# Performance work log

Hardware: AMD Instinct MI355X
Metric: run time of the kernel (lower is better)

The kernel has to match this reference:

```python
import jax, jax.numpy as jnp
import numpy as np

V, E, H, B, L = 50000, 256, 512, 128, 512
T = 9
START, STOP = 7, 8
H2 = H // 2
NEG = -10000.0


def _lstm_dir(x, h0, c0, Wih, Whh, bih, bhh, reverse):
    # x: [B, L, E]; PyTorch gate order i, f, g, o
    def step(carry, xt):
        h, c = carry
        z = xt @ Wih.T + bih + h @ Whh.T + bhh  # [B, 4*H2]
        i, f, g, o = jnp.split(z, 4, axis=-1)
        i = jax.nn.sigmoid(i)
        f = jax.nn.sigmoid(f)
        g = jnp.tanh(g)
        o = jax.nn.sigmoid(o)
        c = f * c + i * g
        h = o * jnp.tanh(c)
        return (h, c), h

    _, hs = jax.lax.scan(step, (h0, c0), x.transpose(1, 0, 2), reverse=reverse)
    return hs.transpose(1, 0, 2)  # [B, L, H2]


def _viterbi(feats, transitions):
    # feats: [B, L, T]; transitions[i, j] = score of j -> i
    alpha0 = jnp.full((B, T), NEG, dtype=feats.dtype).at[:, START].set(0.0)

    def step(alpha, feat):
        # smat[b, prev, nxt] = alpha[b, prev] + feat[b, nxt] + transitions[nxt, prev]
        smat = alpha[:, :, None] + feat[:, None, :] + transitions.T[None]
        return smat.max(axis=1), smat.argmax(axis=1)  # new alpha [B,T], bptr [B,T]

    alpha, backtrace = jax.lax.scan(step, alpha0, feats.transpose(1, 0, 2))  # backtrace: [L, B, T]
    final = alpha + transitions[STOP][None, :]  # [B, T]
    best_score = final.max(axis=1)
    last_tag = final.argmax(axis=1)  # [B]

    def back_step(tag, bptr):
        prev = jnp.take_along_axis(bptr, tag[:, None], axis=1)[:, 0]
        return prev, prev

    # torch loop skips backtrace[0] (points to START)
    _, tags = jax.lax.scan(back_step, last_tag, backtrace[1:], reverse=True)  # [L-1, B]
    path = jnp.concatenate([tags.T, last_tag[:, None]], axis=1)  # [B, L]
    return best_score, path


def setup_inputs():
    key = jax.random.key(0)
    ks = jax.random.split(key, 16)
    s = 0.05
    trans = jax.random.normal(ks[12], (T, T), dtype=jnp.float32)
    trans = trans.at[START, :].set(NEG).at[:, STOP].set(NEG)
    return {
        "tokens": jax.random.randint(ks[0], (B, L), 0, V),
        "embedding": jax.random.normal(ks[1], (V, E), dtype=jnp.float32) * s,
        "Wih_f": jax.random.normal(ks[2], (4 * H2, E), dtype=jnp.float32) * s,
        "Whh_f": jax.random.normal(ks[3], (4 * H2, H2), dtype=jnp.float32) * s,
        "bih_f": jnp.zeros((4 * H2,), dtype=jnp.float32),
        "bhh_f": jnp.zeros((4 * H2,), dtype=jnp.float32),
        "Wih_b": jax.random.normal(ks[4], (4 * H2, E), dtype=jnp.float32) * s,
        "Whh_b": jax.random.normal(ks[5], (4 * H2, H2), dtype=jnp.float32) * s,
        "bih_b": jnp.zeros((4 * H2,), dtype=jnp.float32),
        "bhh_b": jnp.zeros((4 * H2,), dtype=jnp.float32),
        "W_out": jax.random.normal(ks[6], (T, H), dtype=jnp.float32) * s,
        "b_out": jnp.zeros((T,), dtype=jnp.float32),
        "transitions": trans,
        "h0": jax.random.normal(ks[7], (2, B, H2), dtype=jnp.float32),
        "c0": jax.random.normal(ks[8], (2, B, H2), dtype=jnp.float32),
    }


def reference(tokens, embedding, Wih_f, Whh_f, bih_f, bhh_f, Wih_b, Whh_b, bih_b, bhh_b,
              W_out, b_out, transitions, h0, c0):
    x = embedding[tokens]  # [B, L, E]
    hf = _lstm_dir(x, h0[0], c0[0], Wih_f, Whh_f, bih_f, bhh_f, reverse=False)
    hb = _lstm_dir(x, h0[1], c0[1], Wih_b, Whh_b, bih_b, bhh_b, reverse=True)
    lstm_out = jnp.concatenate([hf, hb], axis=-1)  # [B, L, H]
    feats = lstm_out @ W_out.T + b_out  # [B, L, T]
    best_score, path = _viterbi(feats, transitions)
    return best_score, path
```

## Files before the change

kernel.cpp:

```cpp
#include <hip/hip_runtime.h>
#include <hip/hip_bf16.h>
#include <math.h>

#define NB   128
#define LSEQ 512
#define EE   256
#define HH2  256
#define HHH  512
#define TT   9
#define START_TAG 7
#define STOP_TAG  8
#define NEGV -10000.0f

#define ABUF_BYTES 65536
#define ZROW 34
#define LDS_BYTES (ABUF_BYTES + 4 * 32 * ZROW * 4)

#define XFRAG_BYTES  ((size_t)LSEQ * 4 * 16 * 64 * 16)
#define HFRAG_BYTES  ((size_t)LSEQ * 2 * 4 * 16 * 64 * 16)
#define HPLAIN_BYTES ((size_t)LSEQ * NB * HHH * 2)
#define FEATS_BYTES  ((size_t)LSEQ * NB * TT * 4)
#define OFF_HFRAG  XFRAG_BYTES
#define OFF_HPLAIN (OFF_HFRAG + HFRAG_BYTES)
#define OFF_FEATS  (OFF_HPLAIN + HPLAIN_BYTES)
#define OFF_FLAGS  (OFF_FEATS + FEATS_BYTES)

typedef float f32x16 __attribute__((ext_vector_type(16)));
typedef short short8 __attribute__((ext_vector_type(8)));

static __device__ __forceinline__ unsigned short f2bf(float f) {
  unsigned int u = __float_as_uint(f);
  unsigned int r = (u + 0x7fffu + ((u >> 16) & 1u)) >> 16;
  return (unsigned short)r;
}
static __device__ __forceinline__ float bf2f(unsigned short s) {
  return __uint_as_float(((unsigned int)s) << 16);
}
static __device__ __forceinline__ float sigmoidf_(float x) {
  return 1.0f / (1.0f + __expf(-x));
}
static __device__ __forceinline__ float tanhf_(float x) {
  return 2.0f / (1.0f + __expf(-2.0f * x)) - 1.0f;
}

__global__ void init_kernel(unsigned int* flags) {
  if (threadIdx.x < 64) flags[threadIdx.x] = 0u;
}

__global__ void embed_kernel(const int* __restrict__ tokens,
                             const float* __restrict__ emb,
                             uint4* __restrict__ x_frag) {
  int wid = blockIdx.x * blockDim.x + threadIdx.x;
  int l  = wid & 63;
  int ks = (wid >> 6) & 15;
  int bt = (wid >> 10) & 3;
  int t  = wid >> 12;
  int b  = bt * 32 + (l & 31);
  int k  = ks * 16 + (l >> 5) * 8;
  int tok = tokens[b * LSEQ + t];
  const float* p = emb + (size_t)tok * EE + k;
  float4 v0 = *(const float4*)p;
  float4 v1 = *(const float4*)(p + 4);
  uint4 o;
  o.x = f2bf(v0.x) | ((unsigned)f2bf(v0.y) << 16);
  o.y = f2bf(v0.z) | ((unsigned)f2bf(v0.w) << 16);
  o.z = f2bf(v1.x) | ((unsigned)f2bf(v1.y) << 16);
  o.w = f2bf(v1.z) | ((unsigned)f2bf(v1.w) << 16);
  x_frag[wid] = o;
}

__global__ __launch_bounds__(256, 1)
void lstm_kernel(const uint4* __restrict__ x_frag,
                 const float* __restrict__ Wih_f, const float* __restrict__ Whh_f,
                 const float* __restrict__ bih_f, const float* __restrict__ bhh_f,
                 const float* __restrict__ Wih_b, const float* __restrict__ Whh_b,
                 const float* __restrict__ bih_b, const float* __restrict__ bhh_b,
                 const float* __restrict__ h0, const float* __restrict__ c0,
                 uint4* __restrict__ h_frag, ushort* __restrict__ h_plain,
                 unsigned int* __restrict__ flags) {
  extern __shared__ char smem[];
  char*  abuf = smem;
  float* zbuf = (float*)(smem + ABUF_BYTES);

  const int tid  = threadIdx.x;
  const int wv   = tid >> 6;
  const int lane = tid & 63;
  const int d  = blockIdx.x >> 5;
  const int bt = (blockIdx.x >> 3) & 3;
  const int ut = blockIdx.x & 7;
  const int grp = d * 4 + bt;

  const float* Wih = d ? Wih_b : Wih_f;
  const float* Whh = d ? Whh_b : Whh_f;
  const float* bih = d ? bih_b : bih_f;
  const float* bhh = d ? bhh_b : bhh_f;

  short8 w[32];
  {
    int wrow = wv * 256 + ut * 32 + (lane & 31);
#pragma unroll
    for (int ks = 0; ks < 32; ++ks) {
      int k0 = ks * 16 + (lane >> 5) * 8;
      const float* src = (k0 < 256) ? (Wih + (size_t)wrow * 256 + k0)
                                    : (Whh + (size_t)wrow * 256 + (k0 - 256));
      float4 v0 = *(const float4*)src;
      float4 v1 = *(const float4*)(src + 4);
      short8 s;
      s[0] = (short)f2bf(v0.x); s[1] = (short)f2bf(v0.y);
      s[2] = (short)f2bf(v0.z); s[3] = (short)f2bf(v0.w);
      s[4] = (short)f2bf(v1.x); s[5] = (short)f2bf(v1.y);
      s[6] = (short)f2bf(v1.z); s[7] = (short)f2bf(v1.w);
      w[ks] = s;
    }
  }

  const int uj = tid >> 6;
  const int ul = tid & 63;
  const int ubl = ul & 31;
  const int u0l = 16 * uj + 8 * (ul >> 5);
  const int bg  = bt * 32 + ubl;
  const int ug  = ut * 32 + u0l;
  float creg[8];
  float bias[4][8];
  if (tid < 128) {
    const float* cp = c0 + ((size_t)d * NB + bg) * HH2 + ug;
    float4 cv0 = *(const float4*)cp;
    float4 cv1 = *(const float4*)(cp + 4);
    creg[0]=cv0.x; creg[1]=cv0.y; creg[2]=cv0.z; creg[3]=cv0.w;
    creg[4]=cv1.x; creg[5]=cv1.y; creg[6]=cv1.z; creg[7]=cv1.w;
#pragma unroll
    for (int g = 0; g < 4; ++g) {
      int gr = g * 256 + ug;
      float4 a0 = *(const float4*)(bih + gr);
      float4 a1 = *(const float4*)(bih + gr + 4);
      float4 b0 = *(const float4*)(bhh + gr);
      float4 b1 = *(const float4*)(bhh + gr + 4);
      bias[g][0]=a0.x+b0.x; bias[g][1]=a0.y+b0.y; bias[g][2]=a0.z+b0.z; bias[g][3]=a0.w+b0.w;
      bias[g][4]=a1.x+b1.x; bias[g][5]=a1.y+b1.y; bias[g][6]=a1.z+b1.z; bias[g][7]=a1.w+b1.w;
    }
  }

  auto stage_x = [&](int tsrc) {
#pragma unroll
    for (int i = 0; i < 4; ++i) {
      int ks = wv * 4 + i;
      const char* gp = (const char*)x_frag +
          ((((size_t)tsrc * 4 + bt) * 16 + ks) * 64 + lane) * 16;
      char* lp = abuf + (((tsrc & 1) * 32 + ks) * 1024);
      __builtin_amdgcn_global_load_lds(
          (const __attribute__((address_space(1))) unsigned int*)gp,
          (__attribute__((address_space(3))) unsigned int*)lp, 16, 0, 0);
    }
  };
  auto stage_h = [&](int tsrc, int buf) {
#pragma unroll
    for (int i = 0; i < 4; ++i) {
      int ks2 = wv * 4 + i;
      const char* gp = (const char*)h_frag +
          (((((size_t)tsrc * 2 + d) * 4 + bt) * 16 + ks2) * 64 + lane) * 16;
      char* lp = abuf + ((buf * 32 + 16 + ks2) * 1024);
      __builtin_amdgcn_global_load_lds(
          (const __attribute__((address_space(1))) unsigned int*)gp,
          (__attribute__((address_space(3))) unsigned int*)lp, 16, 0, 0);
    }
  };

  stage_x(0);
#pragma unroll
  for (int w2 = 0; w2 < 4; ++w2) {
    int wid = w2 * 256 + tid;
    int ks2 = wid >> 6;
    int l2  = wid & 63;
    int u   = ks2 * 16 + (l2 >> 5) * 8;
    int b2  = bt * 32 + (l2 & 31);
    const float* p = h0 + ((size_t)d * NB + b2) * HH2 + u;
    float4 v0 = *(const float4*)p;
    float4 v1 = *(const float4*)(p + 4);
    uint4 o;
    o.x = f2bf(v0.x) | ((unsigned)f2bf(v0.y) << 16);
    o.y = f2bf(v0.z) | ((unsigned)f2bf(v0.w) << 16);
    o.z = f2bf(v1.x) | ((unsigned)f2bf(v1.y) << 16);
    o.w = f2bf(v1.z) | ((unsigned)f2bf(v1.w) << 16);
    *(uint4*)(abuf + ((16 + ks2) * 1024) + l2 * 16) = o;
  }
  asm volatile("s_waitcnt vmcnt(0)" ::: "memory");
  __syncthreads();

  for (int t = 0; t < LSEQ; ++t) {
    const int cur = t & 1;
    if (t + 1 < LSEQ) stage_x(t + 1);
    if (t > 0) {
      const unsigned int tgt = (unsigned int)t;
      while (true) {
        unsigned int v = __hip_atomic_load(&flags[grp * 8 + (tid & 7)],
                                           __ATOMIC_RELAXED, __HIP_MEMORY_SCOPE_AGENT);
        if (__all(v >= tgt)) break;
        __builtin_amdgcn_s_sleep(1);
      }
      stage_h(t - 1, cur);
    }

    f32x16 acc0, acc1;
#pragma unroll
    for (int i = 0; i < 16; ++i) { acc0[i] = 0.0f; acc1[i] = 0.0f; }

#pragma unroll
    for (int ks = 0; ks < 16; ks += 2) {
      short8 a0 = *(const short8*)(abuf + ((cur * 32 + ks) * 1024) + lane * 16);
      short8 a1 = *(const short8*)(abuf + ((cur * 32 + ks + 1) * 1024) + lane * 16);
      asm volatile("v_mfma_f32_32x32x16_bf16 %0, %1, %2, %0"
                   : "+v"(acc0) : "v"(a0), "v"(w[ks]));
      asm volatile("v_mfma_f32_32x32x16_bf16 %0, %1, %2, %0"
                   : "+v"(acc1) : "v"(a1), "v"(w[ks + 1]));
    }
    asm volatile("s_waitcnt vmcnt(0)" ::: "memory");
    __syncthreads();
#pragma unroll
    for (int ks = 16; ks < 32; ks += 2) {
      short8 a0 = *(const short8*)(abuf + ((cur * 32 + ks) * 1024) + lane * 16);
      short8 a1 = *(const short8*)(abuf + ((cur * 32 + ks + 1) * 1024) + lane * 16);
      asm volatile("v_mfma_f32_32x32x16_bf16 %0, %1, %2, %0"
                   : "+v"(acc0) : "v"(a0), "v"(w[ks]));
      asm volatile("v_mfma_f32_32x32x16_bf16 %0, %1, %2, %0"
                   : "+v"(acc1) : "v"(a1), "v"(w[ks + 1]));
    }
#pragma unroll
    for (int i = 0; i < 16; ++i) acc0[i] += acc1[i];

#pragma unroll
    for (int r = 0; r < 16; ++r) {
      int brow = (r & 3) + 8 * (r >> 2) + 4 * (lane >> 5);
      zbuf[(wv * 32 + brow) * ZROW + (lane & 31)] = acc0[r];
    }
    __syncthreads();

    if (tid < 128) {
      float zr[4][8];
#pragma unroll
      for (int g = 0; g < 4; ++g) {
        const float* zp = zbuf + (g * 32 + ubl) * ZROW + u0l;
        float2 p0 = *(const float2*)zp;
        float2 p1 = *(const float2*)(zp + 2);
        float2 p2 = *(const float2*)(zp + 4);
        float2 p3 = *(const float2*)(zp + 6);
        zr[g][0]=p0.x; zr[g][1]=p0.y; zr[g][2]=p1.x; zr[g][3]=p1.y;
        zr[g][4]=p2.x; zr[g][5]=p2.y; zr[g][6]=p3.x; zr[g][7]=p3.y;
      }
      unsigned short hb[8];
#pragma unroll
      for (int e = 0; e < 8; ++e) {
        float ig = sigmoidf_(zr[0][e] + bias[0][e]);
        float fg = sigmoidf_(zr[1][e] + bias[1][e]);
        float gg = tanhf_   (zr[2][e] + bias[2][e]);
        float og = sigmoidf_(zr[3][e] + bias[3][e]);
        float c = fg * creg[e] + ig * gg;
        creg[e] = c;
        hb[e] = f2bf(og * tanhf_(c));
      }
      int tt = d ? (LSEQ - 1 - t) : t;
      size_t fo = ((((size_t)tt * 2 + d) * 4 + bt) * 16 + (2 * ut + uj)) * 64 + ul;
      unsigned long long w0 = (unsigned long long)(hb[0] | ((unsigned)hb[1] << 16)) |
                              ((unsigned long long)(hb[2] | ((unsigned)hb[3] << 16)) << 32);
      unsigned long long w1 = (unsigned long long)(hb[4] | ((unsigned)hb[5] << 16)) |
                              ((unsigned long long)(hb[6] | ((unsigned)hb[7] << 16)) << 32);
      unsigned long long* fp = (unsigned long long*)((char*)h_frag + fo * 16);
      __hip_atomic_store(fp,     w0, __ATOMIC_RELAXED, __HIP_MEMORY_SCOPE_AGENT);
      __hip_atomic_store(fp + 1, w1, __ATOMIC_RELAXED, __HIP_MEMORY_SCOPE_AGENT);
      uint4 hp;
      hp.x = hb[0] | ((unsigned)hb[1] << 16);
      hp.y = hb[2] | ((unsigned)hb[3] << 16);
      hp.z = hb[4] | ((unsigned)hb[5] << 16);
      hp.w = hb[6] | ((unsigned)hb[7] << 16);
      *(uint4*)(h_plain + (((size_t)tt * NB + bg) * HHH) + d * HH2 + ug) = hp;
    }
    asm volatile("s_waitcnt vmcnt(0)" ::: "memory");
    __syncthreads();
    if (tid == 0)
      __hip_atomic_store(&flags[grp * 8 + ut], (unsigned int)(t + 1),
                         __ATOMIC_RELAXED, __HIP_MEMORY_SCOPE_AGENT);
  }
}

__global__ __launch_bounds__(256)
void feats_kernel(const ushort* __restrict__ h_plain,
                  const float* __restrict__ W_out, const float* __restrict__ b_out,
                  float* __restrict__ feats) {
  int wv = threadIdx.x >> 6, lane = threadIdx.x & 63;
  int wid = blockIdx.x * 4 + wv;
  const ushort* hrow = h_plain + (size_t)wid * HHH + lane * 8;
  uint4 hv = *(const uint4*)hrow;
  float hf[8];
  hf[0] = __uint_as_float(hv.x << 16); hf[1] = __uint_as_float(hv.x & 0xffff0000u);
  hf[2] = __uint_as_float(hv.y << 16); hf[3] = __uint_as_float(hv.y & 0xffff0000u);
  hf[4] = __uint_as_float(hv.z << 16); hf[5] = __uint_as_float(hv.z & 0xffff0000u);
  hf[6] = __uint_as_float(hv.w << 16); hf[7] = __uint_as_float(hv.w & 0xffff0000u);
#pragma unroll
  for (int tg = 0; tg < TT; ++tg) {
    const float* wrow = W_out + (size_t)tg * HHH + lane * 8;
    float4 w0 = *(const float4*)wrow;
    float4 w1 = *(const float4*)(wrow + 4);
    float s = hf[0]*w0.x + hf[1]*w0.y + hf[2]*w0.z + hf[3]*w0.w
            + hf[4]*w1.x + hf[5]*w1.y + hf[6]*w1.z + hf[7]*w1.w;
#pragma unroll
    for (int off = 32; off >= 1; off >>= 1) s += __shfl_xor(s, off);
    if (lane == 0) feats[(size_t)wid * TT + tg] = s + b_out[tg];
  }
}

__global__ __launch_bounds__(64)
void viterbi_kernel(const float* __restrict__ feats, const float* __restrict__ trans,
                    float* __restrict__ out) {
  __shared__ float tr[TT * TT];
  __shared__ float abuf2[2][16];
  __shared__ int   bptr[LSEQ][TT];
  __shared__ float finbuf[16];
  int b = blockIdx.x, lane = threadIdx.x;
  for (int i = lane; i < TT * TT; i += 64) tr[i] = trans[i];
  if (lane < 16) abuf2[0][lane] = NEGV;
  __syncthreads();
  if (lane == START_TAG) abuf2[0][lane] = 0.f;
  int cur = 0;
  for (int l = 0; l < LSEQ; ++l) {
    float feat = (lane < TT) ? feats[((size_t)l * NB + b) * TT + lane] : 0.f;
    if (lane < TT) {
      float best = -3.4e38f; int bp = 0;
#pragma unroll
      for (int p = 0; p < TT; ++p) {
        float s2 = abuf2[cur][p] + tr[lane * TT + p];
        if (s2 > best) { best = s2; bp = p; }
      }
      abuf2[cur ^ 1][lane] = best + feat;
      bptr[l][lane] = bp;
    }
    cur ^= 1;
  }
  if (lane < 16) finbuf[lane] = -3.4e38f;
  if (lane < TT) finbuf[lane] = abuf2[cur][lane] + tr[STOP_TAG * TT + lane];
  if (lane == 0) {
    float bestv = finbuf[0]; int btag = 0;
    for (int p = 1; p < TT; ++p) if (finbuf[p] > bestv) { bestv = finbuf[p]; btag = p; }
    out[b] = bestv;
    float* pathp = out + NB + (size_t)b * LSEQ;
    int tag = btag;
    pathp[LSEQ - 1] = (float)tag;
    for (int l = LSEQ - 1; l >= 1; --l) {
      tag = bptr[l][tag];
      pathp[l - 1] = (float)tag;
    }
  }
}

extern "C" void kernel_launch(void* const* d_in, const int* in_sizes, int n_in,
                              void* d_out, int out_size, void* d_ws, size_t ws_size,
                              hipStream_t stream) {
  const int*   tokens = (const int*)d_in[0];
  const float* emb    = (const float*)d_in[1];
  const float* Wih_f  = (const float*)d_in[2];
  const float* Whh_f  = (const float*)d_in[3];
  const float* bih_f  = (const float*)d_in[4];
  const float* bhh_f  = (const float*)d_in[5];
  const float* Wih_b  = (const float*)d_in[6];
  const float* Whh_b  = (const float*)d_in[7];
  const float* bih_b  = (const float*)d_in[8];
  const float* bhh_b  = (const float*)d_in[9];
  const float* W_out  = (const float*)d_in[10];
  const float* b_out  = (const float*)d_in[11];
  const float* trans  = (const float*)d_in[12];
  const float* h0     = (const float*)d_in[13];
  const float* c0     = (const float*)d_in[14];
  float* out = (float*)d_out;

  char* ws = (char*)d_ws;
  uint4* x_frag  = (uint4*)ws;
  uint4* h_frag  = (uint4*)(ws + OFF_HFRAG);
  ushort* h_plain = (ushort*)(ws + OFF_HPLAIN);
  float* feats   = (float*)(ws + OFF_FEATS);
  unsigned int* flags = (unsigned int*)(ws + OFF_FLAGS);

  hipFuncSetAttribute((const void*)lstm_kernel,
                      hipFuncAttributeMaxDynamicSharedMemorySize, LDS_BYTES);

  init_kernel<<<1, 64, 0, stream>>>(flags);
  embed_kernel<<<(LSEQ * 4 * 16 * 64) / 256, 256, 0, stream>>>(tokens, emb, x_frag);
  lstm_kernel<<<64, 256, LDS_BYTES, stream>>>(x_frag, Wih_f, Whh_f, bih_f, bhh_f,
                                              Wih_b, Whh_b, bih_b, bhh_b,
                                              h0, c0, h_frag, h_plain, flags);
  feats_kernel<<<(LSEQ * NB) / 4, 256, 0, stream>>>(h_plain, W_out, b_out, feats);
  viterbi_kernel<<<NB, 64, 0, stream>>>(feats, trans, out);
}
```

Measured before the change: 2.575 ms.

## Halve LSTM blocks to 32 with 512 threads, fewer cross-block sync participants

The persistent LSTM kernel moves from 64 blocks of 256 threads to 32 blocks of 512 threads. Each block now covers 64 hidden units across all four gates, so every direction and batch group waits on 4 peer blocks per step instead of 8. Only one wave polls the flags, followed by a block barrier, and the h staging buffer is now single-buffered. The aim is to lower per-timestep grid synchronisation latency. The cost is an extra __syncthreads per step and fewer CUs doing the per-step matmul work.

```diff
diff --git a/kernel.cpp b/kernel.cpp
--- a/kernel.cpp
+++ b/kernel.cpp
@@ -12,9 +12,11 @@
 #define STOP_TAG  8
 #define NEGV -10000.0f
 
-#define ABUF_BYTES 65536
-#define ZROW 34
-#define LDS_BYTES (ABUF_BYTES + 4 * 32 * ZROW * 4)
+#define XBUF_BYTES 32768
+#define HBUF_OFF   XBUF_BYTES
+#define ZBUF_OFF   (XBUF_BYTES + 16384)
+#define ZROW 66
+#define LDS_BYTES (ZBUF_OFF + 4 * 32 * ZROW * 4)
 
 #define XFRAG_BYTES  ((size_t)LSEQ * 4 * 16 * 64 * 16)
 #define HFRAG_BYTES  ((size_t)LSEQ * 2 * 4 * 16 * 64 * 16)
@@ -24,6 +26,7 @@
 #define OFF_HPLAIN (OFF_HFRAG + HFRAG_BYTES)
 #define OFF_FEATS  (OFF_HPLAIN + HPLAIN_BYTES)
 #define OFF_FLAGS  (OFF_FEATS + FEATS_BYTES)
+#define FLAG_UINTS 128
 
 typedef float f32x16 __attribute__((ext_vector_type(16)));
 typedef short short8 __attribute__((ext_vector_type(8)));
@@ -33,9 +36,6 @@
   unsigned int r = (u + 0x7fffu + ((u >> 16) & 1u)) >> 16;
   return (unsigned short)r;
 }
-static __device__ __forceinline__ float bf2f(unsigned short s) {
-  return __uint_as_float(((unsigned int)s) << 16);
-}
 static __device__ __forceinline__ float sigmoidf_(float x) {
   return 1.0f / (1.0f + __expf(-x));
 }
@@ -44,7 +44,7 @@
 }
 
 __global__ void init_kernel(unsigned int* flags) {
-  if (threadIdx.x < 64) flags[threadIdx.x] = 0u;
+  if (threadIdx.x < FLAG_UINTS) flags[threadIdx.x] = 0u;
 }
 
 __global__ void embed_kernel(const int* __restrict__ tokens,
@@ -69,7 +69,7 @@
   x_frag[wid] = o;
 }
 
-__global__ __launch_bounds__(256, 1)
+__global__ __launch_bounds__(512, 2)
 void lstm_kernel(const uint4* __restrict__ x_frag,
                  const float* __restrict__ Wih_f, const float* __restrict__ Whh_f,
                  const float* __restrict__ bih_f, const float* __restrict__ bhh_f,
@@ -80,14 +80,16 @@
                  unsigned int* __restrict__ flags) {
   extern __shared__ char smem[];
   char*  abuf = smem;
-  float* zbuf = (float*)(smem + ABUF_BYTES);
+  float* zbuf = (float*)(smem + ZBUF_OFF);
 
   const int tid  = threadIdx.x;
   const int wv   = tid >> 6;
   const int lane = tid & 63;
-  const int d  = blockIdx.x >> 5;
-  const int bt = (blockIdx.x >> 3) & 3;
-  const int ut = blockIdx.x & 7;
+  const int gate = wv >> 1;
+  const int uh   = wv & 1;
+  const int d  = blockIdx.x >> 4;
+  const int bt = (blockIdx.x >> 2) & 3;
+  const int ut = blockIdx.x & 3;
   const int grp = d * 4 + bt;
 
   const float* Wih = d ? Wih_b : Wih_f;
@@ -97,7 +99,7 @@
 
   short8 w[32];
   {
-    int wrow = wv * 256 + ut * 32 + (lane & 31);
+    int wrow = gate * 256 + ut * 64 + uh * 32 + (lane & 31);
 #pragma unroll
     for (int ks = 0; ks < 32; ++ks) {
       int k0 = ks * 16 + (lane >> 5) * 8;
@@ -114,15 +116,13 @@
     }
   }
 
-  const int uj = tid >> 6;
-  const int ul = tid & 63;
-  const int ubl = ul & 31;
-  const int u0l = 16 * uj + 8 * (ul >> 5);
-  const int bg  = bt * 32 + ubl;
-  const int ug  = ut * 32 + u0l;
+  const int ub  = tid & 31;
+  const int un8 = tid >> 5;
+  const int bg  = bt * 32 + ub;
+  const int ug  = ut * 64 + un8 * 8;
   float creg[8];
   float bias[4][8];
-  if (tid < 128) {
+  if (tid < 256) {
     const float* cp = c0 + ((size_t)d * NB + bg) * HH2 + ug;
     float4 cv0 = *(const float4*)cp;
     float4 cv1 = *(const float4*)(cp + 4);
@@ -142,23 +142,23 @@
 
   auto stage_x = [&](int tsrc) {
 #pragma unroll
-    for (int i = 0; i < 4; ++i) {
-      int ks = wv * 4 + i;
+    for (int i = 0; i < 2; ++i) {
+      int ks = wv * 2 + i;
       const char* gp = (const char*)x_frag +
           ((((size_t)tsrc * 4 + bt) * 16 + ks) * 64 + lane) * 16;
-      char* lp = abuf + (((tsrc & 1) * 32 + ks) * 1024);
+      char* lp = abuf + (tsrc & 1) * 16384 + ks * 1024;
       __builtin_amdgcn_global_load_lds(
           (const __attribute__((address_space(1))) unsigned int*)gp,
           (__attribute__((address_space(3))) unsigned int*)lp, 16, 0, 0);
     }
   };
-  auto stage_h = [&](int tsrc, int buf) {
-#pragma unroll
-    for (int i = 0; i < 4; ++i) {
-      int ks2 = wv * 4 + i;
+  auto stage_h = [&](int tsrc) {
+#pragma unroll
+    for (int i = 0; i < 2; ++i) {
+      int ks = wv * 2 + i;
       const char* gp = (const char*)h_frag +
-          (((((size_t)tsrc * 2 + d) * 4 + bt) * 16 + ks2) * 64 + lane) * 16;
-      char* lp = abuf + ((buf * 32 + 16 + ks2) * 1024);
+          (((((size_t)tsrc * 2 + d) * 4 + bt) * 16 + ks) * 64 + lane) * 16;
+      char* lp = abuf + HBUF_OFF + ks * 1024;
       __builtin_amdgcn_global_load_lds(
           (const __attribute__((address_space(1))) unsigned int*)gp,
           (__attribute__((address_space(3))) unsigned int*)lp, 16, 0, 0);
@@ -167,8 +167,8 @@
 
   stage_x(0);
 #pragma unroll
-  for (int w2 = 0; w2 < 4; ++w2) {
-    int wid = w2 * 256 + tid;
+  for (int w2 = 0; w2 < 2; ++w2) {
+    int wid = w2 * 512 + tid;
     int ks2 = wid >> 6;
     int l2  = wid & 63;
     int u   = ks2 * 16 + (l2 >> 5) * 8;
@@ -181,7 +181,7 @@
     o.y = f2bf(v0.z) | ((unsigned)f2bf(v0.w) << 16);
     o.z = f2bf(v1.x) | ((unsigned)f2bf(v1.y) << 16);
     o.w = f2bf(v1.z) | ((unsigned)f2bf(v1.w) << 16);
-    *(uint4*)(abuf + ((16 + ks2) * 1024) + l2 * 16) = o;
+    *(uint4*)(abuf + HBUF_OFF + ks2 * 1024 + l2 * 16) = o;
   }
   asm volatile("s_waitcnt vmcnt(0)" ::: "memory");
   __syncthreads();
@@ -190,14 +190,17 @@
     const int cur = t & 1;
     if (t + 1 < LSEQ) stage_x(t + 1);
     if (t > 0) {
-      const unsigned int tgt = (unsigned int)t;
-      while (true) {
-        unsigned int v = __hip_atomic_load(&flags[grp * 8 + (tid & 7)],
-                                           __ATOMIC_RELAXED, __HIP_MEMORY_SCOPE_AGENT);
-        if (__all(v >= tgt)) break;
-        __builtin_amdgcn_s_sleep(1);
+      if (wv == 0) {
+        const unsigned int tgt = (unsigned int)t;
+        while (true) {
+          unsigned int v = __hip_atomic_load(&flags[grp * 16 + (lane & 3)],
+                                             __ATOMIC_RELAXED, __HIP_MEMORY_SCOPE_AGENT);
+          if (__all(v >= tgt)) break;
+          __builtin_amdgcn_s_sleep(1);
+        }
       }
-      stage_h(t - 1, cur);
+      __syncthreads();
+      stage_h(t - 1);
     }
 
     f32x16 acc0, acc1;
@@ -206,8 +209,8 @@
 
 #pragma unroll
     for (int ks = 0; ks < 16; ks += 2) {
-      short8 a0 = *(const short8*)(abuf + ((cur * 32 + ks) * 1024) + lane * 16);
-      short8 a1 = *(const short8*)(abuf + ((cur * 32 + ks + 1) * 1024) + lane * 16);
+      short8 a0 = *(const short8*)(abuf + cur * 16384 + ks * 1024 + lane * 16);
+      short8 a1 = *(const short8*)(abuf + cur * 16384 + (ks + 1) * 1024 + lane * 16);
       asm volatile("v_mfma_f32_32x32x16_bf16 %0, %1, %2, %0"
                    : "+v"(acc0) : "v"(a0), "v"(w[ks]));
       asm volatile("v_mfma_f32_32x32x16_bf16 %0, %1, %2, %0"
@@ -217,8 +220,8 @@
     __syncthreads();
 #pragma unroll
     for (int ks = 16; ks < 32; ks += 2) {
-      short8 a0 = *(const short8*)(abuf + ((cur * 32 + ks) * 1024) + lane * 16);
-      short8 a1 = *(const short8*)(abuf + ((cur * 32 + ks + 1) * 1024) + lane * 16);
+      short8 a0 = *(const short8*)(abuf + HBUF_OFF + (ks - 16) * 1024 + lane * 16);
+      short8 a1 = *(const short8*)(abuf + HBUF_OFF + (ks - 15) * 1024 + lane * 16);
       asm volatile("v_mfma_f32_32x32x16_bf16 %0, %1, %2, %0"
                    : "+v"(acc0) : "v"(a0), "v"(w[ks]));
       asm volatile("v_mfma_f32_32x32x16_bf16 %0, %1, %2, %0"
@@ -230,21 +233,19 @@
 #pragma unroll
     for (int r = 0; r < 16; ++r) {
       int brow = (r & 3) + 8 * (r >> 2) + 4 * (lane >> 5);
-      zbuf[(wv * 32 + brow) * ZROW + (lane & 31)] = acc0[r];
+      zbuf[(gate * 32 + brow) * ZROW + uh * 32 + (lane & 31)] = acc0[r];
     }
     __syncthreads();
 
-    if (tid < 128) {
+    if (tid < 256) {
       float zr[4][8];
 #pragma unroll
       for (int g = 0; g < 4; ++g) {
-        const float* zp = zbuf + (g * 32 + ubl) * ZROW + u0l;
-        float2 p0 = *(const float2*)zp;
-        float2 p1 = *(const float2*)(zp + 2);
-        float2 p2 = *(const float2*)(zp + 4);
-        float2 p3 = *(const float2*)(zp + 6);
-        zr[g][0]=p0.x; zr[g][1]=p0.y; zr[g][2]=p1.x; zr[g][3]=p1.y;
-        zr[g][4]=p2.x; zr[g][5]=p2.y; zr[g][6]=p3.x; zr[g][7]=p3.y;
+        const float* zp = zbuf + (g * 32 + ub) * ZROW + un8 * 8;
+        float4 p0 = *(const float4*)zp;
+        float4 p1 = *(const float4*)(zp + 4);
+        zr[g][0]=p0.x; zr[g][1]=p0.y; zr[g][2]=p0.z; zr[g][3]=p0.w;
+        zr[g][4]=p1.x; zr[g][5]=p1.y; zr[g][6]=p1.z; zr[g][7]=p1.w;
       }
       unsigned short hb[8];
 #pragma unroll
@@ -258,7 +259,8 @@
         hb[e] = f2bf(og * tanhf_(c));
       }
       int tt = d ? (LSEQ - 1 - t) : t;
-      size_t fo = ((((size_t)tt * 2 + d) * 4 + bt) * 16 + (2 * ut + uj)) * 64 + ul;
+      size_t fo = ((((size_t)tt * 2 + d) * 4 + bt) * 16 + (ut * 4 + (un8 >> 1))) * 64
+                + ((un8 & 1) * 32 + ub);
       unsigned long long w0 = (unsigned long long)(hb[0] | ((unsigned)hb[1] << 16)) |
                               ((unsigned long long)(hb[2] | ((unsigned)hb[3] << 16)) << 32);
       unsigned long long w1 = (unsigned long long)(hb[4] | ((unsigned)hb[5] << 16)) |
@@ -272,11 +274,11 @@
       hp.z = hb[4] | ((unsigned)hb[5] << 16);
       hp.w = hb[6] | ((unsigned)hb[7] << 16);
       *(uint4*)(h_plain + (((size_t)tt * NB + bg) * HHH) + d * HH2 + ug) = hp;
-    }
-    asm volatile("s_waitcnt vmcnt(0)" ::: "memory");
+      asm volatile("s_waitcnt vmcnt(0)" ::: "memory");
+    }
     __syncthreads();
     if (tid == 0)
-      __hip_atomic_store(&flags[grp * 8 + ut], (unsigned int)(t + 1),
+      __hip_atomic_store(&flags[grp * 16 + ut], (unsigned int)(t + 1),
                          __ATOMIC_RELAXED, __HIP_MEMORY_SCOPE_AGENT);
   }
 }
@@ -380,9 +382,9 @@
   hipFuncSetAttribute((const void*)lstm_kernel,
                       hipFuncAttributeMaxDynamicSharedMemorySize, LDS_BYTES);
 
-  init_kernel<<<1, 64, 0, stream>>>(flags);
+  init_kernel<<<1, 128, 0, stream>>>(flags);
   embed_kernel<<<(LSEQ * 4 * 16 * 64) / 256, 256, 0, stream>>>(tokens, emb, x_frag);
-  lstm_kernel<<<64, 256, LDS_BYTES, stream>>>(x_frag, Wih_f, Whh_f, bih_f, bhh_f,
+  lstm_kernel<<<32, 512, LDS_BYTES, stream>>>(x_frag, Wih_f, Whh_f, bih_f, bhh_f,
                                               Wih_b, Whh_b, bih_b, bhh_b,
                                               h0, c0, h_frag, h_plain, flags);
   feats_kernel<<<(LSEQ * NB) / 4, 256, 0, stream>>>(h_plain, W_out, b_out, feats);
```

Result: slower. 2.648 ms (+2.8%).
